# Kernel tuning notes

Measured on AMD Instinct MI355X. Metric: run time of the kernel, lower is better.

The kernel has to match this reference:

```python
import jax, jax.numpy as jnp
import numpy as np

# Network topology constants (topological order: inputs, L hidden layers, outputs)
N_IN = 512
H = 1024      # hidden nodes per layer
L = 8         # hidden layers
N_OUT = 256
DEG = 64      # enabled incoming connections per non-input node
B = 1024      # batch of input vectors

LAYER_SIZES = [H] * L + [N_OUT]
E_TOTAL = sum(n * DEG for n in LAYER_SIZES)  # 540672


def setup_inputs() -> dict:
    key = jax.random.key(0)
    k_in, k_w = jax.random.split(key)
    inputs = jax.random.normal(k_in, (B, N_IN), dtype=jnp.float32)
    # scale weights ~1/sqrt(DEG) so sigmoid pre-activations are well-conditioned
    weights = jax.random.normal(k_w, (E_TOTAL,), dtype=jnp.float32) / np.sqrt(DEG)
    # src indices: for each layer, incoming edges may come from ANY earlier node
    rng = np.random.default_rng(0)
    src_chunks = []
    n_before = N_IN
    for n in LAYER_SIZES:
        src_chunks.append(rng.integers(0, n_before, size=n * DEG))
        n_before += n
    src_idx = jnp.asarray(np.concatenate(src_chunks), dtype=jnp.int32)
    return {"inputs": inputs, "weights": weights, "src_idx": src_idx}


def reference(inputs, weights, src_idx):
    # outs: [B, n_nodes_evaluated_so_far], grown layer by layer (topological order)
    outs = inputs
    off = 0
    for n in LAYER_SIZES:
        e = n * DEG
        s = src_idx[off:off + e]            # [e] gather indices into earlier nodes
        w = weights[off:off + e]            # [e]
        gathered = outs[:, s] * w           # [B, e] irregular gather + scale
        z = gathered.reshape(-1, n, DEG).sum(-1)  # per-node sum over DEG in-edges
        outs = jnp.concatenate([outs, jax.nn.sigmoid(z)], axis=1)
        off += e
    return outs[:, -N_OUT:]  # [B, N_OUT] outputs of 'output' nodes
```

## Files before the change

### kernel.cpp

```cpp
#include <hip/hip_runtime.h>
#include <math.h>


#define N_IN    512
#define NLAYER  9
#define DEG     64
#define BATCH   1024
#define BPB     4
#define THREADS 1024
#define TOTAL_N 8960
#define N_OUT   256
#define NREC    135168

__device__ __forceinline__ unsigned f2bf(float f) {
    unsigned u = __float_as_uint(f);
    return (u + 0x7fffu + ((u >> 16) & 1u)) >> 16;
}
__device__ __forceinline__ float bflo(unsigned u) { return __uint_as_float(u << 16); }
__device__ __forceinline__ float bfhi(unsigned u) { return __uint_as_float(u & 0xffff0000u); }

__global__ __launch_bounds__(256)
void neat_prep(const float* __restrict__ wts,
               const int*   __restrict__ sidx,
               uint4*       __restrict__ rec)
{
    int r = blockIdx.x * 256 + threadIdx.x;
    if (r >= NREC) return;
    int l = r >> 14;
    int j = r & 16383;
    int n = ((j >> 10) << 6) | (j & 63);
    int q = (j >> 6) & 15;
    int e0 = (l << 16) + (n << 6) + (q << 2);
    int4   s4 = *reinterpret_cast<const int4*>(sidx + e0);
    float4 w4 = *reinterpret_cast<const float4*>(wts + e0);
    uint4 o;
    o.x = (unsigned)s4.x | ((unsigned)s4.y << 16);
    o.y = (unsigned)s4.z | ((unsigned)s4.w << 16);
    o.z = f2bf(w4.x) | (f2bf(w4.y) << 16);
    o.w = f2bf(w4.z) | (f2bf(w4.w) << 16);
    rec[r] = o;
}

__global__ __launch_bounds__(THREADS, 4)
void neat_fwd(const float* __restrict__ in,
              const uint4* __restrict__ rec,
              float*       __restrict__ out)
{
    __shared__ unsigned short act[TOTAL_N * BPB];

    const int tid   = threadIdx.x;
    const int bbase = blockIdx.x * BPB;

    {
        const float* src = in + bbase * N_IN;
        for (int t = tid; t < BPB * N_IN; t += THREADS) {
            int j = t >> 9;
            int i = t & (N_IN - 1);
            act[i * BPB + j] = (unsigned short)f2bf(src[t]);
        }
    }
    __syncthreads();

    int recBase = 0;
    int nb      = N_IN;
    #pragma unroll 1
    for (int layer = 0; layer < NLAYER; ++layer) {
        const int n = (layer < NLAYER - 1) ? 1024 : N_OUT;
        for (int neuron = tid; neuron < n; neuron += THREADS) {
            const uint4* rp = rec + recBase + ((neuron >> 6) << 10) + (neuron & 63);

            float4 acc = make_float4(0.f, 0.f, 0.f, 0.f);
            #pragma unroll 4
            for (int q = 0; q < DEG / 4; ++q) {
                const uint4 r4 = rp[q << 6];
                const uint2 g0 = *reinterpret_cast<const uint2*>(act + ((r4.x & 0xffffu) << 2));
                const uint2 g1 = *reinterpret_cast<const uint2*>(act + ((r4.x >> 16) << 2));
                const uint2 g2 = *reinterpret_cast<const uint2*>(act + ((r4.y & 0xffffu) << 2));
                const uint2 g3 = *reinterpret_cast<const uint2*>(act + ((r4.y >> 16) << 2));
                const float w0 = bflo(r4.z), w1 = bfhi(r4.z);
                const float w2 = bflo(r4.w), w3 = bfhi(r4.w);
                acc.x += bflo(g0.x)*w0 + bflo(g1.x)*w1 + bflo(g2.x)*w2 + bflo(g3.x)*w3;
                acc.y += bfhi(g0.x)*w0 + bfhi(g1.x)*w1 + bfhi(g2.x)*w2 + bfhi(g3.x)*w3;
                acc.z += bflo(g0.y)*w0 + bflo(g1.y)*w1 + bflo(g2.y)*w2 + bflo(g3.y)*w3;
                acc.w += bfhi(g0.y)*w0 + bfhi(g1.y)*w1 + bfhi(g2.y)*w2 + bfhi(g3.y)*w3;
            }

            float4 sg;
            sg.x = 1.f / (1.f + __expf(-acc.x));
            sg.y = 1.f / (1.f + __expf(-acc.y));
            sg.z = 1.f / (1.f + __expf(-acc.z));
            sg.w = 1.f / (1.f + __expf(-acc.w));

            if (layer < NLAYER - 1) {
                uint2 p;
                p.x = f2bf(sg.x) | (f2bf(sg.y) << 16);
                p.y = f2bf(sg.z) | (f2bf(sg.w) << 16);
                *reinterpret_cast<uint2*>(act + ((nb + neuron) << 2)) = p;
            } else {
                float* op = out + neuron;
                op[(bbase + 0) * N_OUT] = sg.x;
                op[(bbase + 1) * N_OUT] = sg.y;
                op[(bbase + 2) * N_OUT] = sg.z;
                op[(bbase + 3) * N_OUT] = sg.w;
            }
        }
        __syncthreads();
        recBase += n << 4;
        nb      += n;
    }
}

extern "C" void kernel_launch(void* const* d_in, const int* in_sizes, int n_in,
                              void* d_out, int out_size, void* d_ws, size_t ws_size,
                              hipStream_t stream)
{
    const float* in  = (const float*)d_in[0];
    const float* wts = (const float*)d_in[1];
    const int*   sx  = (const int*)d_in[2];
    float*       out = (float*)d_out;
    uint4*       rec = (uint4*)d_ws;

    neat_prep<<<(NREC + 255) / 256, 256, 0, stream>>>(wts, sx, rec);
    neat_fwd<<<BATCH / BPB, THREADS, 0, stream>>>(in, rec, out);
}
```

Measured before the change: 58.78 us.

## Reorder per-neuron edges by LDS bank and switch activations to fp16

The prep kernel now bins each neuron's 64 incoming edges by source index modulo 16 and rotates the slot order by the lane id. The aim is for the lanes of a wavefront that gather activations at the same step to hit different LDS banks, which reduces bank conflicts in the forward gather. Activations and weights are also stored as fp16 rather than bf16, which uses native half conversions instead of manual bit manipulation but changes numeric precision and range. The prep kernel now runs only 132 blocks of 64 threads with serial per-thread loops, so it may take longer itself.

```diff
diff --git a/kernel.cpp b/kernel.cpp
--- a/kernel.cpp
+++ b/kernel.cpp
@@ -10,35 +10,50 @@
 #define THREADS 1024
 #define TOTAL_N 8960
 #define N_OUT   256
-#define NREC    135168
+#define NGROUP  132
+#define NREC    (NGROUP * 1024)
 
-__device__ __forceinline__ unsigned f2bf(float f) {
-    unsigned u = __float_as_uint(f);
-    return (u + 0x7fffu + ((u >> 16) & 1u)) >> 16;
-}
-__device__ __forceinline__ float bflo(unsigned u) { return __uint_as_float(u << 16); }
-__device__ __forceinline__ float bfhi(unsigned u) { return __uint_as_float(u & 0xffff0000u); }
+union H4 { uint2 u; _Float16 h[4]; };
+union H2 { unsigned u; _Float16 h[2]; };
+union HS { _Float16 h; unsigned short s; };
 
-__global__ __launch_bounds__(256)
+__global__ __launch_bounds__(64)
 void neat_prep(const float* __restrict__ wts,
                const int*   __restrict__ sidx,
                uint4*       __restrict__ rec)
 {
-    int r = blockIdx.x * 256 + threadIdx.x;
-    if (r >= NREC) return;
-    int l = r >> 14;
-    int j = r & 16383;
-    int n = ((j >> 10) << 6) | (j & 63);
-    int q = (j >> 6) & 15;
-    int e0 = (l << 16) + (n << 6) + (q << 2);
-    int4   s4 = *reinterpret_cast<const int4*>(sidx + e0);
-    float4 w4 = *reinterpret_cast<const float4*>(wts + e0);
-    uint4 o;
-    o.x = (unsigned)s4.x | ((unsigned)s4.y << 16);
-    o.y = (unsigned)s4.z | ((unsigned)s4.w << 16);
-    o.z = f2bf(w4.x) | (f2bf(w4.y) << 16);
-    o.w = f2bf(w4.z) | (f2bf(w4.w) << 16);
-    rec[r] = o;
+    __shared__ int            sbin[64][16];
+    __shared__ unsigned short srec[64 * 16 * 8];
+
+    const int t = threadIdx.x;
+    const int g = blockIdx.x;
+    const int layer = (g < 128) ? (g >> 4) : 8;
+    const int nloc  = (g < 128) ? ((g & 15) << 6) + t : ((g - 128) << 6) + t;
+    const int eoff  = (layer << 16) + (nloc << 6);
+
+    #pragma unroll
+    for (int b = 0; b < 16; ++b) sbin[t][b] = 0;
+
+    for (int e = 0; e < DEG; ++e) sbin[t][sidx[eoff + e] & 15]++;
+
+    int run = 0;
+    #pragma unroll
+    for (int b = 0; b < 16; ++b) { int c = sbin[t][b]; sbin[t][b] = run; run += c; }
+
+    for (int e = 0; e < DEG; ++e) {
+        const int idx = sidx[eoff + e];
+        const int p   = sbin[t][idx & 15]++;
+        const int slot = (p - t) & 63;
+        const int q = slot >> 2, gg = slot & 3;
+        HS w; w.h = (_Float16)wts[eoff + e];
+        srec[(t * 16 + q) * 8 + gg]     = (unsigned short)idx;
+        srec[(t * 16 + q) * 8 + 4 + gg] = w.s;
+    }
+    __syncthreads();
+
+    const uint4* sr = reinterpret_cast<const uint4*>(srec);
+    for (int q = 0; q < 16; ++q)
+        rec[(g << 10) + (q << 6) + t] = sr[t * 16 + q];
 }
 
 __global__ __launch_bounds__(THREADS, 4)
@@ -46,7 +61,7 @@
               const uint4* __restrict__ rec,
               float*       __restrict__ out)
 {
-    __shared__ unsigned short act[TOTAL_N * BPB];
+    __shared__ _Float16 act[TOTAL_N * BPB];
 
     const int tid   = threadIdx.x;
     const int bbase = blockIdx.x * BPB;
@@ -56,7 +71,7 @@
         for (int t = tid; t < BPB * N_IN; t += THREADS) {
             int j = t >> 9;
             int i = t & (N_IN - 1);
-            act[i * BPB + j] = (unsigned short)f2bf(src[t]);
+            act[i * BPB + j] = (_Float16)src[t];
         }
     }
     __syncthreads();
@@ -73,16 +88,28 @@
             #pragma unroll 4
             for (int q = 0; q < DEG / 4; ++q) {
                 const uint4 r4 = rp[q << 6];
-                const uint2 g0 = *reinterpret_cast<const uint2*>(act + ((r4.x & 0xffffu) << 2));
-                const uint2 g1 = *reinterpret_cast<const uint2*>(act + ((r4.x >> 16) << 2));
-                const uint2 g2 = *reinterpret_cast<const uint2*>(act + ((r4.y & 0xffffu) << 2));
-                const uint2 g3 = *reinterpret_cast<const uint2*>(act + ((r4.y >> 16) << 2));
-                const float w0 = bflo(r4.z), w1 = bfhi(r4.z);
-                const float w2 = bflo(r4.w), w3 = bfhi(r4.w);
-                acc.x += bflo(g0.x)*w0 + bflo(g1.x)*w1 + bflo(g2.x)*w2 + bflo(g3.x)*w3;
-                acc.y += bfhi(g0.x)*w0 + bfhi(g1.x)*w1 + bfhi(g2.x)*w2 + bfhi(g3.x)*w3;
-                acc.z += bflo(g0.y)*w0 + bflo(g1.y)*w1 + bflo(g2.y)*w2 + bflo(g3.y)*w3;
-                acc.w += bfhi(g0.y)*w0 + bfhi(g1.y)*w1 + bfhi(g2.y)*w2 + bfhi(g3.y)*w3;
+                H4 g0, g1, g2, g3;
+                g0.u = *reinterpret_cast<const uint2*>(act + ((r4.x & 0xffffu) << 2));
+                g1.u = *reinterpret_cast<const uint2*>(act + ((r4.x >> 16) << 2));
+                g2.u = *reinterpret_cast<const uint2*>(act + ((r4.y & 0xffffu) << 2));
+                g3.u = *reinterpret_cast<const uint2*>(act + ((r4.y >> 16) << 2));
+                H2 wz, ww; wz.u = r4.z; ww.u = r4.w;
+                acc.x += (float)g0.h[0] * (float)wz.h[0];
+                acc.y += (float)g0.h[1] * (float)wz.h[0];
+                acc.z += (float)g0.h[2] * (float)wz.h[0];
+                acc.w += (float)g0.h[3] * (float)wz.h[0];
+                acc.x += (float)g1.h[0] * (float)wz.h[1];
+                acc.y += (float)g1.h[1] * (float)wz.h[1];
+                acc.z += (float)g1.h[2] * (float)wz.h[1];
+                acc.w += (float)g1.h[3] * (float)wz.h[1];
+                acc.x += (float)g2.h[0] * (float)ww.h[0];
+                acc.y += (float)g2.h[1] * (float)ww.h[0];
+                acc.z += (float)g2.h[2] * (float)ww.h[0];
+                acc.w += (float)g2.h[3] * (float)ww.h[0];
+                acc.x += (float)g3.h[0] * (float)ww.h[1];
+                acc.y += (float)g3.h[1] * (float)ww.h[1];
+                acc.z += (float)g3.h[2] * (float)ww.h[1];
+                acc.w += (float)g3.h[3] * (float)ww.h[1];
             }
 
             float4 sg;
@@ -92,10 +119,10 @@
             sg.w = 1.f / (1.f + __expf(-acc.w));
 
             if (layer < NLAYER - 1) {
-                uint2 p;
-                p.x = f2bf(sg.x) | (f2bf(sg.y) << 16);
-                p.y = f2bf(sg.z) | (f2bf(sg.w) << 16);
-                *reinterpret_cast<uint2*>(act + ((nb + neuron) << 2)) = p;
+                H4 p;
+                p.h[0] = (_Float16)sg.x; p.h[1] = (_Float16)sg.y;
+                p.h[2] = (_Float16)sg.z; p.h[3] = (_Float16)sg.w;
+                *reinterpret_cast<uint2*>(act + ((nb + neuron) << 2)) = p.u;
             } else {
                 float* op = out + neuron;
                 op[(bbase + 0) * N_OUT] = sg.x;
@@ -120,6 +147,6 @@
     float*       out = (float*)d_out;
     uint4*       rec = (uint4*)d_ws;
 
-    neat_prep<<<(NREC + 255) / 256, 256, 0, stream>>>(wts, sx, rec);
+    neat_prep<<<NGROUP, 64, 0, stream>>>(wts, sx, rec);
     neat_fwd<<<BATCH / BPB, THREADS, 0, stream>>>(in, rec, out);
 }
```

New measurement: 63.75 us. 8.5% more time.
